# Kernel optimization log

Measured on AMD Instinct MI355X. Metric: run time of the kernel, lower is better.

The kernel has to match this reference:

```python
import jax, jax.numpy as jnp
import numpy as np

B, S, D = 4, 1024, 1024
H, HD = 16, 64
MAXPOS = 1024  # max_position_embeddings


def setup_inputs() -> dict:
    key = jax.random.key(0)
    ks = jax.random.split(key, 10)
    sc = 0.02
    return {
        "hidden_states": jax.random.normal(ks[0], (B, S, D), dtype=jnp.float32),
        "attention_mask": jnp.zeros((B, 1, 1, S), dtype=jnp.float32),
        "across_attention_prior": jax.random.uniform(ks[1], (B, H, S, S), dtype=jnp.float32),
        "head_mask": jnp.ones((1, H, 1, 1), dtype=jnp.float32),
        "Wq": jax.random.normal(ks[2], (D, D), dtype=jnp.float32) * sc,
        "bq": jnp.zeros((D,), dtype=jnp.float32),
        "Wk": jax.random.normal(ks[3], (D, D), dtype=jnp.float32) * sc,
        "bk": jnp.zeros((D,), dtype=jnp.float32),
        "Wv": jax.random.normal(ks[4], (D, D), dtype=jnp.float32) * sc,
        "bv": jnp.zeros((D,), dtype=jnp.float32),
        "dist_emb": jax.random.normal(ks[5], (2 * MAXPOS - 1, HD), dtype=jnp.float32) * sc,
    }


def _heads(x):
    # [B,S,D] -> [B,H,S,HD]
    return x.reshape(B, S, H, HD).transpose(0, 2, 1, 3)


def reference(hidden_states, attention_mask, across_attention_prior, head_mask,
              Wq, bq, Wk, bk, Wv, bv, dist_emb):
    q = _heads(hidden_states @ Wq + bq)  # [B,H,S,HD]
    k = _heads(hidden_states @ Wk + bk)
    v = _heads(hidden_states @ Wv + bv)

    scores = jnp.einsum("bhld,bhrd->bhlr", q, k)

    # relative_key_query positional bias
    pos = jnp.arange(S)
    distance = pos[:, None] - pos[None, :]  # [S,S]
    pe = dist_emb[distance + MAXPOS - 1]  # [S,S,HD] (l, r, d)
    scores = scores + jnp.einsum("bhld,lrd->bhlr", q, pe)
    scores = scores + jnp.einsum("bhrd,lrd->bhlr", k, pe)

    scores = scores / jnp.sqrt(jnp.float32(HD))
    scores = scores + attention_mask  # additive mask, broadcast [B,1,1,S]

    probs = jax.nn.softmax(scores, axis=-1)
    probs = probs * across_attention_prior  # post-softmax multiplicative prior
    probs = probs * head_mask  # dropout prob = 0 (eval)

    ctx = jnp.einsum("bhlr,bhrd->bhld", probs, v)
    ctx = ctx.transpose(0, 2, 1, 3).reshape(B, S, D)
    return ctx
```

## Files before the change

kernel.cpp:

```cpp
#include <hip/hip_runtime.h>


typedef unsigned short u16;
typedef unsigned int   u32;
typedef __attribute__((ext_vector_type(8))) short bfx8;
typedef __attribute__((ext_vector_type(4))) float f32x4;
typedef __attribute__((ext_vector_type(4))) unsigned short u16x4;

#define MFMA_BF16(a, b, c) __builtin_amdgcn_mfma_f32_16x16x32_bf16(a, b, c, 0, 0, 0)

__device__ __forceinline__ u16 f2bf(float f) {
    union { float f; u32 u; } c; c.f = f;
    u32 u = c.u;
    return (u16)((u + 0x7FFFu + ((u >> 16) & 1u)) >> 16);
}
__device__ __forceinline__ float bf2f(u16 v) {
    union { u32 u; float f; } c; c.u = ((u32)v) << 16;
    return c.f;
}
__device__ __forceinline__ float load_f(const void* p, long i, bool bf) {
    return bf ? bf2f(((const u16*)p)[i]) : ((const float*)p)[i];
}
__device__ __forceinline__ u16 load_bf(const void* p, long i, bool bf) {
    return bf ? ((const u16*)p)[i] : f2bf(((const float*)p)[i]);
}

__device__ __forceinline__ void gload16(const u16* g, u16* l) {
    __builtin_amdgcn_global_load_lds(
        (__attribute__((address_space(1))) void*)g,
        (__attribute__((address_space(3))) void*)l, 16, 0, 0);
}

__device__ __forceinline__ void wg_barrier() {
    asm volatile("s_waitcnt lgkmcnt(0)" ::: "memory");
    __builtin_amdgcn_s_barrier();
    asm volatile("" ::: "memory");
}

__global__ void k_detect(const u32* hid, int* flags) {
    __shared__ int cnt;
    if (threadIdx.x == 0) cnt = 0;
    __syncthreads();
    int c = 0;
    for (int i = threadIdx.x; i < 1024; i += 256) {
        u32 w = hid[i];
        u32 e = (w >> 7) & 0xFFu;
        if (e >= 100u && e <= 140u) c++;
    }
    atomicAdd(&cnt, c);
    __syncthreads();
    if (threadIdx.x == 0) flags[0] = (cnt > 512) ? 1 : 0;
}

__global__ void k_prep(const void* hidden, const void* dist, const void* mask,
                       const void* hm, const void* bq, const void* bk,
                       const void* bv, const int* flags, u16* hid_bf,
                       u16* dist_bf, float* mask_f, float* hm_f, float* bias_f) {
    const bool bf = flags[0] != 0;
    const long NH = 4L * 1024 * 1024, ND = 2047L * 64, NM = 4096, NB = 3072, NHM = 16;
    const long TOT = NH + ND + NM + NB + NHM;
    for (long i = (long)blockIdx.x * 256 + threadIdx.x; i < TOT;
         i += (long)gridDim.x * 256) {
        if (i < NH) hid_bf[i] = load_bf(hidden, i, bf);
        else if (i < NH + ND) dist_bf[i - NH] = load_bf(dist, i - NH, bf);
        else if (i < NH + ND + NM) mask_f[i - NH - ND] = load_f(mask, i - NH - ND, bf);
        else if (i < NH + ND + NM + NB) {
            long j = i - NH - ND - NM;
            const void* src = (j < 1024) ? bq : ((j < 2048) ? bk : bv);
            bias_f[j] = load_f(src, j & 1023, bf);
        } else {
            long j = i - NH - ND - NM - NB;
            hm_f[j] = load_f(hm, j, bf);
        }
    }
}

__global__ void k_transpose(const void* Wq, const void* Wk, const void* Wv,
                            const int* flags, u16* wt) {
    const bool bf = flags[0] != 0;
    __shared__ float t[32][33];
    const int z = blockIdx.z;
    const void* W = (z == 0) ? Wq : ((z == 1) ? Wk : Wv);
    int x = blockIdx.x * 32 + threadIdx.x;
    for (int i = 0; i < 4; i++) {
        int y = blockIdx.y * 32 + threadIdx.y + i * 8;
        t[threadIdx.y + i * 8][threadIdx.x] = load_f(W, (long)y * 1024 + x, bf);
    }
    __syncthreads();
    int x2 = blockIdx.y * 32 + threadIdx.x;
    u16* out = wt + (long)z * 1024 * 1024;
    for (int i = 0; i < 4; i++) {
        int y2 = blockIdx.x * 32 + threadIdx.y + i * 8;
        out[(long)y2 * 1024 + x2] = f2bf(t[threadIdx.x][threadIdx.y + i * 8]);
    }
}

__global__ __launch_bounds__(256, 2)
void k_qkv_gemm(const u16* A, const u16* Bt, const float* bias,
                u16* qb, u16* kb, u16* vb) {
    __shared__ u16 sA[128 * 64];
    __shared__ u16 sB[128 * 64];
    const int tid = threadIdx.x;
    const int w = tid >> 6, lane = tid & 63;
    const int quad = lane >> 4, nl = lane & 15;
    const int wr = w >> 1, wc = w & 1;
    const int bid0 = blockIdx.y * 24 + blockIdx.x;
    const int bid = (bid0 & 7) * 96 + (bid0 >> 3);
    const int n0 = (bid % 24) * 128, m0 = (bid / 24) * 128;

    f32x4 acc[4][4];
#pragma unroll
    for (int a = 0; a < 4; a++)
#pragma unroll
        for (int b = 0; b < 4; b++) acc[a][b] = (f32x4){0.f, 0.f, 0.f, 0.f};

    const int srow = 32 * w + (lane >> 3);
    const int seg = lane & 7;

    for (int kt = 0; kt < 16; kt++) {
        const int k0 = kt * 64;
        __syncthreads();
#pragma unroll
        for (int j = 0; j < 4; j++) {
            int row = srow + 8 * j;
            int ss = (seg ^ (row & 7)) * 8;
            gload16(A + (long)(m0 + row) * 1024 + k0 + ss, sA + (32 * w + 8 * j) * 64);
            gload16(Bt + (long)(n0 + row) * 1024 + k0 + ss, sB + (32 * w + 8 * j) * 64);
        }
        __syncthreads();

        bfx8 af[4][2], bfr[4][2];
#pragma unroll
        for (int f = 0; f < 4; f++) {
#pragma unroll
            for (int hh = 0; hh < 2; hh++) {
                int Ra = 64 * wr + 16 * f + nl;
                int Rb = 64 * wc + 16 * f + nl;
                af[f][hh]  = *(const bfx8*)(sA + Ra * 64 + (((4 * hh + quad) ^ (Ra & 7)) * 8));
                bfr[f][hh] = *(const bfx8*)(sB + Rb * 64 + (((4 * hh + quad) ^ (Rb & 7)) * 8));
            }
        }
#pragma unroll
        for (int fm = 0; fm < 4; fm++)
#pragma unroll
            for (int fn = 0; fn < 4; fn++) {
                acc[fm][fn] = MFMA_BF16(af[fm][0], bfr[fn][0], acc[fm][fn]);
                acc[fm][fn] = MFMA_BF16(af[fm][1], bfr[fn][1], acc[fm][fn]);
            }
    }

#pragma unroll
    for (int fm = 0; fm < 4; fm++) {
#pragma unroll
        for (int fn = 0; fn < 4; fn++) {
            int n = n0 + 64 * wc + 16 * fn + nl;
            int which = n >> 10, hcol = n & 1023;
            int h = hcol >> 6, hd = hcol & 63;
            u16* op = (which == 0) ? qb : ((which == 1) ? kb : vb);
            float bias_v = bias[n];
#pragma unroll
            for (int reg = 0; reg < 4; reg++) {
                int m = m0 + 64 * wr + 16 * fm + 4 * quad + reg;
                int b = m >> 10, s = m & 1023;
                float v = acc[fm][fn][reg] + bias_v;
                op[((long)((b * 16 + h) * 1024 + s)) * 64 + hd] = f2bf(v);
            }
        }
    }
}

__global__ __launch_bounds__(512, 4)
void k_attn(const u16* qb, const u16* kb, const u16* vb, const u16* Eb,
            const float* maskf, const float* hmf, const void* prior,
            const int* flags, void* out) {
    constexpr int PT = 72;
    constexpr int PD = 132;
    constexpr int PX = 66;
    __shared__ __align__(16) char smem[79872];
    u16* sQ  = (u16*)(smem);
    u16* sK  = (u16*)(smem + 9216);
    u16* sVT = (u16*)(smem + 18432);
    u16* sE  = (u16*)(smem + 27648);
    u16* sDq = (u16*)(smem + 46080);
    u16* sDk = (u16*)(smem + 62976);
    u16* sP  = (u16*)(smem + 46080);
    float* accx = (float*)(smem + 46080);
    float* zs   = (float*)(smem + 9216);

    const int tid = threadIdx.x;
    const int W = tid >> 6, lane = tid & 63;
    const int s = W >> 1, c = W & 1;
    const int quad = lane >> 4, nl = lane & 15;
    const int bh = blockIdx.x, b = bh >> 4, h = bh & 15;
    const int l0 = blockIdx.y * 64;
    const bool bf = flags[0] != 0;

    const u16* qbh = qb + (long)bh * 65536;
    const u16* kbh = kb + (long)bh * 65536;
    const u16* vbh = vb + (long)bh * 65536;

    {
        int row = tid >> 3, s8 = tid & 7;
        *(int4*)(sQ + row * PT + s8 * 8) = *(const int4*)(qbh + (l0 + row) * 64 + s8 * 8);
    }

    const int erow = tid >> 3, es8 = tid & 7;
    const int jb_base = l0 + 960;

    int4 nK0, nE0, nE1, nV0;
    {
        nK0 = *(const int4*)(kbh + erow * 64 + es8 * 8);
        int j0 = jb_base + erow;       if (j0 > 2046) j0 = 2046;
        int j1 = jb_base + 64 + erow;  if (j1 > 2046) j1 = 2046;
        nE0 = *(const int4*)(Eb + (long)j0 * 64 + es8 * 8);
        nE1 = *(const int4*)(Eb + (long)j1 * 64 + es8 * 8);
        nV0 = *(const int4*)(vbh + lane * 64 + W * 8);
    }

    wg_barrier();
    const bfx8 aq0 = *(const bfx8*)(sQ + (16 * s + nl) * PT + quad * 8);
    const bfx8 aq1 = *(const bfx8*)(sQ + (16 * s + nl) * PT + quad * 8 + 32);

    f32x4 accv[4];
#pragma unroll
    for (int f = 0; f < 4; f++) accv[f] = (f32x4){0.f, 0.f, 0.f, 0.f};
    float zrow = 0.f;

    for (int it = 0; it < 16; it++) {
        const int r0 = it * 64;
        wg_barrier();

        *(int4*)(sK + erow * PT + es8 * 8)        = nK0;
        *(int4*)(sE + erow * PT + es8 * 8)        = nE0;
        *(int4*)(sE + (64 + erow) * PT + es8 * 8) = nE1;
        {
            const u16* pv = (const u16*)&nV0;
#pragma unroll
            for (int j2 = 0; j2 < 8; j2++) sVT[(W * 8 + j2) * PT + lane] = pv[j2];
        }

        f32x4 mvec[2], prv[2];
#pragma unroll
        for (int f2 = 0; f2 < 2; f2++) {
            const int colr = r0 + 32 * c + 16 * f2 + 4 * quad;
            mvec[f2] = *(const f32x4*)(maskf + b * 1024 + colr);
            long prow = ((long)(bh * 1024 + l0 + 16 * s + nl)) * 1024 + colr;
            if (bf) {
                u16x4 t = *(const u16x4*)((const u16*)prior + prow);
                prv[f2] = (f32x4){bf2f(t[0]), bf2f(t[1]), bf2f(t[2]), bf2f(t[3])};
            } else {
                prv[f2] = *(const f32x4*)((const float*)prior + prow);
            }
        }

        if (it < 15) {
            const int r0n = r0 + 64;
            const int jbn = jb_base - r0n;
            nK0 = *(const int4*)(kbh + (r0n + erow) * 64 + es8 * 8);
            int j0 = jbn + erow;       if (j0 > 2046) j0 = 2046;
            int j1 = jbn + 64 + erow;  if (j1 > 2046) j1 = 2046;
            nE0 = *(const int4*)(Eb + (long)j0 * 64 + es8 * 8);
            nE1 = *(const int4*)(Eb + (long)j1 * 64 + es8 * 8);
            nV0 = *(const int4*)(vbh + (r0n + lane) * 64 + W * 8);
        }
        wg_barrier();

        const bfx8 ak0 = *(const bfx8*)(sK + (16 * s + nl) * PT + quad * 8);
        const bfx8 ak1 = *(const bfx8*)(sK + (16 * s + nl) * PT + quad * 8 + 32);

#pragma unroll
        for (int fcl = 0; fcl < 4; fcl++) {
            const int ub = (4 * c + fcl) * 16;
            const int R = ub + nl;
            bfx8 be0 = *(const bfx8*)(sE + R * PT + quad * 8);
            bfx8 be1 = *(const bfx8*)(sE + R * PT + quad * 8 + 32);
            f32x4 dq = (f32x4){0.f, 0.f, 0.f, 0.f};
            dq = MFMA_BF16(be0, aq0, dq);
            dq = MFMA_BF16(be1, aq1, dq);
            u16x4 dqp;
#pragma unroll
            for (int reg = 0; reg < 4; reg++) dqp[reg] = f2bf(dq[reg]);
            *(u16x4*)(sDq + (16 * s + nl) * PD + ub + 4 * quad) = dqp;
            f32x4 dk = (f32x4){0.f, 0.f, 0.f, 0.f};
            dk = MFMA_BF16(ak0, be0, dk);
            dk = MFMA_BF16(ak1, be1, dk);
#pragma unroll
            for (int reg = 0; reg < 4; reg++)
                sDk[(16 * s + 4 * quad + reg) * PD + ub + nl] = f2bf(dk[reg]);
        }
        f32x4 accs[2];
#pragma unroll
        for (int f2 = 0; f2 < 2; f2++) {
            const int R = (2 * c + f2) * 16 + nl;
            bfx8 ka0 = *(const bfx8*)(sK + R * PT + quad * 8);
            bfx8 ka1 = *(const bfx8*)(sK + R * PT + quad * 8 + 32);
            f32x4 sv = (f32x4){0.f, 0.f, 0.f, 0.f};
            sv = MFMA_BF16(ka0, aq0, sv);
            sv = MFMA_BF16(ka1, aq1, sv);
            accs[f2] = sv;
        }
        wg_barrier();

        u16x4 pw4[2];
        const int li = 16 * s + nl;
#pragma unroll
        for (int f2 = 0; f2 < 2; f2++) {
#pragma unroll
            for (int reg = 0; reg < 4; reg++) {
                int ri = (2 * c + f2) * 16 + 4 * quad + reg;
                int u = li - ri + 63;
                float sv = (accs[f2][reg] + bf2f(sDq[li * PD + u])
                            + bf2f(sDk[ri * PD + u])) * 0.125f + mvec[f2][reg];
                float e = __expf(sv);
                zrow += e;
                pw4[f2][reg] = f2bf(e * prv[f2][reg]);
            }
        }
        wg_barrier();

#pragma unroll
        for (int f2 = 0; f2 < 2; f2++)
            *(u16x4*)(sP + li * PT + 32 * c + 16 * f2 + 4 * quad) = pw4[f2];

        const bfx8 ap = *(const bfx8*)(sP + li * PT + 32 * c + quad * 8);
#pragma unroll
        for (int fd = 0; fd < 4; fd++) {
            bfx8 bv = *(const bfx8*)(sVT + (fd * 16 + nl) * PT + 32 * c + quad * 8);
            accv[fd] = MFMA_BF16(ap, bv, accv[fd]);
        }
    }

    zrow += __shfl_xor(zrow, 16);
    zrow += __shfl_xor(zrow, 32);

    wg_barrier();
    if (c == 1) {
#pragma unroll
        for (int fd = 0; fd < 4; fd++)
#pragma unroll
            for (int reg = 0; reg < 4; reg++)
                accx[(16 * s + 4 * quad + reg) * PX + fd * 16 + nl] = accv[fd][reg];
    }
    if (quad == 0) zs[(16 * s + nl) * 2 + c] = zrow;
    wg_barrier();
    if (c == 0) {
        const float hm = hmf[h];
        float zt[4];
#pragma unroll
        for (int reg = 0; reg < 4; reg++) {
            int li2 = 16 * s + 4 * quad + reg;
            zt[reg] = zs[li2 * 2] + zs[li2 * 2 + 1];
        }
#pragma unroll
        for (int fd = 0; fd < 4; fd++) {
#pragma unroll
            for (int reg = 0; reg < 4; reg++) {
                int li2 = 16 * s + 4 * quad + reg;
                int d = fd * 16 + nl;
                float val = (accv[fd][reg] + accx[li2 * PX + fd * 16 + nl]) * hm / zt[reg];
                long oidx = ((long)(b * 1024 + l0 + li2)) * 1024 + h * 64 + d;
                if (bf) ((u16*)out)[oidx] = f2bf(val);
                else    ((float*)out)[oidx] = val;
            }
        }
    }
}

extern "C" void kernel_launch(void* const* d_in, const int* in_sizes, int n_in,
                              void* d_out, int out_size, void* d_ws, size_t ws_size,
                              hipStream_t stream) {
    char* ws = (char*)d_ws;
    int*   flags   = (int*)ws;
    u16*   hid_bf  = (u16*)(ws + 256);
    u16*   wt_bf   = (u16*)(ws + 8388864);
    u16*   dist_bf = (u16*)(ws + 14680320);
    float* mask_f  = (float*)(ws + 14942464);
    float* bias_f  = (float*)(ws + 14958848);
    float* hm_f    = (float*)(ws + 14971136);
    u16*   q_bf    = (u16*)(ws + 14971392);
    u16*   k_bf    = (u16*)(ws + 23360000);
    u16*   v_bf    = (u16*)(ws + 31748608);

    k_detect<<<1, 256, 0, stream>>>((const u32*)d_in[0], flags);
    k_prep<<<2048, 256, 0, stream>>>(d_in[0], d_in[10], d_in[1], d_in[3],
                                     d_in[5], d_in[7], d_in[9], flags,
                                     hid_bf, dist_bf, mask_f, hm_f, bias_f);
    k_transpose<<<dim3(32, 32, 3), dim3(32, 8), 0, stream>>>(
        d_in[4], d_in[6], d_in[8], flags, wt_bf);
    k_qkv_gemm<<<dim3(24, 32), 256, 0, stream>>>(hid_bf, wt_bf, bias_f,
                                                 q_bf, k_bf, v_bf);
    k_attn<<<dim3(64, 16), 512, 0, stream>>>(q_bf, k_bf, v_bf, dist_bf,
                                             mask_f, hm_f, d_in[2], flags, d_out);
}
```

Measured before the change: 511.5 us.

## Skip unused relative-position tiles, alias sP onto sE, vectorize prep, tune GEMM

The attention kernel now computes only the diagonal bands of the Q·E and K·E products that the score gather actually reads, and skips the rest of the 8 column tiles per wave. sP moves to alias the sE buffer instead of sDq, which lets one barrier per iteration be dropped. The prep kernel converts hidden states and distance embeddings 8 elements per thread with 16-byte stores, with no grid-stride loop. The QKV GEMM raises its occupancy hint to 3 and interleaves LDS fragment loads with MFMAs per k-half to reduce register pressure. Risks are a wrong band range or an LDS race from the removed barrier, and a prep kernel that now relies on the launch grid exactly covering the data.

```diff
diff --git a/kernel.cpp b/kernel.cpp
--- a/kernel.cpp
+++ b/kernel.cpp
@@ -20,9 +20,6 @@
 }
 __device__ __forceinline__ float load_f(const void* p, long i, bool bf) {
     return bf ? bf2f(((const u16*)p)[i]) : ((const float*)p)[i];
-}
-__device__ __forceinline__ u16 load_bf(const void* p, long i, bool bf) {
-    return bf ? ((const u16*)p)[i] : f2bf(((const float*)p)[i]);
 }
 
 __device__ __forceinline__ void gload16(const u16* g, u16* l) {
@@ -57,22 +54,34 @@
                        const void* bv, const int* flags, u16* hid_bf,
                        u16* dist_bf, float* mask_f, float* hm_f, float* bias_f) {
     const bool bf = flags[0] != 0;
-    const long NH = 4L * 1024 * 1024, ND = 2047L * 64, NM = 4096, NB = 3072, NHM = 16;
-    const long TOT = NH + ND + NM + NB + NHM;
-    for (long i = (long)blockIdx.x * 256 + threadIdx.x; i < TOT;
-         i += (long)gridDim.x * 256) {
-        if (i < NH) hid_bf[i] = load_bf(hidden, i, bf);
-        else if (i < NH + ND) dist_bf[i - NH] = load_bf(dist, i - NH, bf);
-        else if (i < NH + ND + NM) mask_f[i - NH - ND] = load_f(mask, i - NH - ND, bf);
-        else if (i < NH + ND + NM + NB) {
-            long j = i - NH - ND - NM;
-            const void* src = (j < 1024) ? bq : ((j < 2048) ? bk : bv);
-            bias_f[j] = load_f(src, j & 1023, bf);
+    const long tid = (long)blockIdx.x * 256 + threadIdx.x;
+
+    if (bf) {
+        ((int4*)hid_bf)[tid] = ((const int4*)hidden)[tid];
+    } else {
+        const float* hf = (const float*)hidden + tid * 8;
+        int4 o; u16* op = (u16*)&o;
+#pragma unroll
+        for (int j = 0; j < 8; j++) op[j] = f2bf(hf[j]);
+        ((int4*)hid_bf)[tid] = o;
+    }
+    if (tid < 16376) {
+        if (bf) {
+            ((int4*)dist_bf)[tid] = ((const int4*)dist)[tid];
         } else {
-            long j = i - NH - ND - NM - NB;
-            hm_f[j] = load_f(hm, j, bf);
-        }
-    }
+            const float* df = (const float*)dist + tid * 8;
+            int4 o; u16* op = (u16*)&o;
+#pragma unroll
+            for (int j = 0; j < 8; j++) op[j] = f2bf(df[j]);
+            ((int4*)dist_bf)[tid] = o;
+        }
+    }
+    if (tid < 4096) mask_f[tid] = load_f(mask, tid, bf);
+    if (tid < 3072) {
+        const void* src = (tid < 1024) ? bq : ((tid < 2048) ? bk : bv);
+        bias_f[tid] = load_f(src, tid & 1023, bf);
+    }
+    if (tid < 16) hm_f[tid] = load_f(hm, tid, bf);
 }
 
 __global__ void k_transpose(const void* Wq, const void* Wk, const void* Wv,
@@ -95,7 +104,7 @@
     }
 }
 
-__global__ __launch_bounds__(256, 2)
+__global__ __launch_bounds__(256, 3)
 void k_qkv_gemm(const u16* A, const u16* Bt, const float* bias,
                 u16* qb, u16* kb, u16* vb) {
     __shared__ u16 sA[128 * 64];
@@ -129,24 +138,22 @@
         }
         __syncthreads();
 
-        bfx8 af[4][2], bfr[4][2];
-#pragma unroll
-        for (int f = 0; f < 4; f++) {
-#pragma unroll
-            for (int hh = 0; hh < 2; hh++) {
+#pragma unroll
+        for (int hh = 0; hh < 2; hh++) {
+            bfx8 af[4], bfr[4];
+#pragma unroll
+            for (int f = 0; f < 4; f++) {
                 int Ra = 64 * wr + 16 * f + nl;
                 int Rb = 64 * wc + 16 * f + nl;
-                af[f][hh]  = *(const bfx8*)(sA + Ra * 64 + (((4 * hh + quad) ^ (Ra & 7)) * 8));
-                bfr[f][hh] = *(const bfx8*)(sB + Rb * 64 + (((4 * hh + quad) ^ (Rb & 7)) * 8));
-            }
-        }
-#pragma unroll
-        for (int fm = 0; fm < 4; fm++)
-#pragma unroll
-            for (int fn = 0; fn < 4; fn++) {
-                acc[fm][fn] = MFMA_BF16(af[fm][0], bfr[fn][0], acc[fm][fn]);
-                acc[fm][fn] = MFMA_BF16(af[fm][1], bfr[fn][1], acc[fm][fn]);
-            }
+                af[f]  = *(const bfx8*)(sA + Ra * 64 + (((4 * hh + quad) ^ (Ra & 7)) * 8));
+                bfr[f] = *(const bfx8*)(sB + Rb * 64 + (((4 * hh + quad) ^ (Rb & 7)) * 8));
+            }
+#pragma unroll
+            for (int fm = 0; fm < 4; fm++)
+#pragma unroll
+                for (int fn = 0; fn < 4; fn++)
+                    acc[fm][fn] = MFMA_BF16(af[fm], bfr[fn], acc[fm][fn]);
+        }
     }
 
 #pragma unroll
@@ -181,9 +188,9 @@
     u16* sK  = (u16*)(smem + 9216);
     u16* sVT = (u16*)(smem + 18432);
     u16* sE  = (u16*)(smem + 27648);
+    u16* sP  = (u16*)(smem + 27648);
     u16* sDq = (u16*)(smem + 46080);
     u16* sDk = (u16*)(smem + 62976);
-    u16* sP  = (u16*)(smem + 46080);
     float* accx = (float*)(smem + 46080);
     float* zs   = (float*)(smem + 9216);
 
@@ -220,6 +227,9 @@
     wg_barrier();
     const bfx8 aq0 = *(const bfx8*)(sQ + (16 * s + nl) * PT + quad * 8);
     const bfx8 aq1 = *(const bfx8*)(sQ + (16 * s + nl) * PT + quad * 8 + 32);
+
+    const int dql = c ? s + 3 : s,     dqh = c ? s + 4 : s + 2;
+    const int dkl = c ? 6 - s : 3 - s, dkh = c ? 7 - s : 5 - s;
 
     f32x4 accv[4];
 #pragma unroll
@@ -269,24 +279,31 @@
         const bfx8 ak1 = *(const bfx8*)(sK + (16 * s + nl) * PT + quad * 8 + 32);
 
 #pragma unroll
-        for (int fcl = 0; fcl < 4; fcl++) {
-            const int ub = (4 * c + fcl) * 16;
+        for (int fc = 0; fc < 8; fc++) {
+            const bool uq = (fc >= dql) && (fc <= dqh);
+            const bool uk = (fc >= dkl) && (fc <= dkh);
+            if (!(uq || uk)) continue;
+            const int ub = fc * 16;
             const int R = ub + nl;
             bfx8 be0 = *(const bfx8*)(sE + R * PT + quad * 8);
             bfx8 be1 = *(const bfx8*)(sE + R * PT + quad * 8 + 32);
-            f32x4 dq = (f32x4){0.f, 0.f, 0.f, 0.f};
-            dq = MFMA_BF16(be0, aq0, dq);
-            dq = MFMA_BF16(be1, aq1, dq);
-            u16x4 dqp;
-#pragma unroll
-            for (int reg = 0; reg < 4; reg++) dqp[reg] = f2bf(dq[reg]);
-            *(u16x4*)(sDq + (16 * s + nl) * PD + ub + 4 * quad) = dqp;
-            f32x4 dk = (f32x4){0.f, 0.f, 0.f, 0.f};
-            dk = MFMA_BF16(ak0, be0, dk);
-            dk = MFMA_BF16(ak1, be1, dk);
-#pragma unroll
-            for (int reg = 0; reg < 4; reg++)
-                sDk[(16 * s + 4 * quad + reg) * PD + ub + nl] = f2bf(dk[reg]);
+            if (uq) {
+                f32x4 dq = (f32x4){0.f, 0.f, 0.f, 0.f};
+                dq = MFMA_BF16(be0, aq0, dq);
+                dq = MFMA_BF16(be1, aq1, dq);
+                u16x4 dqp;
+#pragma unroll
+                for (int reg = 0; reg < 4; reg++) dqp[reg] = f2bf(dq[reg]);
+                *(u16x4*)(sDq + (16 * s + nl) * PD + ub + 4 * quad) = dqp;
+            }
+            if (uk) {
+                f32x4 dk = (f32x4){0.f, 0.f, 0.f, 0.f};
+                dk = MFMA_BF16(ak0, be0, dk);
+                dk = MFMA_BF16(ak1, be1, dk);
+#pragma unroll
+                for (int reg = 0; reg < 4; reg++)
+                    sDk[(16 * s + 4 * quad + reg) * PD + ub + nl] = f2bf(dk[reg]);
+            }
         }
         f32x4 accs[2];
 #pragma unroll
@@ -316,7 +333,6 @@
                 pw4[f2][reg] = f2bf(e * prv[f2][reg]);
             }
         }
-        wg_barrier();
 
 #pragma unroll
         for (int f2 = 0; f2 < 2; f2++)
```

Measured after the change: 499.8 us. 1.02x faster.
